# Performance work log

Measured on AMD Instinct MI355X. Metric: run time of the kernel, lower is better.

## Reference

```python
import jax, jax.numpy as jnp
from jax import lax
import numpy as np


def _bn(x, g, b, eps=1e-5):
    # BatchNorm2d in training mode: biased batch stats over (N,H,W) per channel
    m = jnp.mean(x, axis=(0, 2, 3), keepdims=True)
    v = jnp.mean((x - m) ** 2, axis=(0, 2, 3), keepdims=True)
    return (x - m) * lax.rsqrt(v + eps) * g[None, :, None, None] + b[None, :, None, None]


def _conv(x, w, b, pad):
    y = lax.conv_general_dilated(x, w, (1, 1), [(pad, pad), (pad, pad)],
                                 dimension_numbers=('NCHW', 'OIHW', 'NCHW'))
    return y + b[None, :, None, None]


def _prelu(x, a):
    return jnp.where(x >= 0, x, a * x)


def _maxpool2(x):
    return lax.reduce_window(x, -jnp.inf, lax.max, (1, 1, 2, 2), (1, 1, 2, 2), 'VALID')


def _up2(x):
    # UpsamplingBilinear2d(scale_factor=2) -> bilinear, align_corners=True
    B, C, H, W = x.shape
    def idx(n):
        pos = jnp.arange(2 * n, dtype=x.dtype) * (n - 1) / (2 * n - 1)
        lo = jnp.floor(pos).astype(jnp.int32)
        hi = jnp.minimum(lo + 1, n - 1)
        return lo, hi, pos - lo.astype(x.dtype)
    lo, hi, f = idx(H)
    x = x[:, :, lo, :] * (1 - f)[:, None] + x[:, :, hi, :] * f[:, None]
    lo, hi, f = idx(W)
    x = x[:, :, :, lo] * (1 - f) + x[:, :, :, hi] * f
    return x


def _forward(x, n16, sigma16, bias16, prelu_a,
             bn3_g, bn3_b, bn32_g, bn32_b, bn64_g, bn64_b, bn128_g, bn128_b,
             w1, b1, w2, b2, w3, b3, w4, b4, w5, b5, w6, b6, w7, b7, w11, b11):
    B, C, H, W = x.shape
    # 16 enhancement curves fused: r_k = x^{n_k} / (x^{n_k} + sigma_k^{n_k} + bias_k)
    xn = x[None] ** n16[:, None, None, None, None]          # (16,B,3,H,W)
    r = xn / (xn + (sigma16 ** n16)[:, None, None, None, None]
              + bias16[:, None, None, None, None])
    # each branch gets its own BatchNorm2d(3) stats (same affine params)
    r = jax.vmap(lambda t: _bn(t, bn3_g, bn3_b))(r)
    x_fusion = jnp.transpose(r, (1, 0, 2, 3, 4)).reshape(B, 16 * C, H, W)
    x1 = _bn(_maxpool2(_prelu(_conv(x_fusion, w1, b1, 1), prelu_a)), bn32_g, bn32_b)
    x2 = _bn(_maxpool2(_prelu(_conv(x1, w2, b2, 1), prelu_a)), bn64_g, bn64_b)
    x3 = _bn(_maxpool2(_prelu(_conv(x2, w3, b3, 1), prelu_a)), bn128_g, bn128_b)
    x4 = _bn(_conv(x3, w4, b4, 1), bn128_g, bn128_b)
    x5 = _bn(_up2(_prelu(_conv(jnp.concatenate([x4, x3], 1), w5, b5, 1), prelu_a)), bn64_g, bn64_b)
    x6 = _bn(_up2(_prelu(_conv(jnp.concatenate([x2, x5], 1), w6, b6, 1), prelu_a)), bn32_g, bn32_b)
    x_out = jax.nn.sigmoid(_up2(_prelu(_conv(jnp.concatenate([x1, x6], 1), w7, b7, 1), prelu_a)))
    x_out = _conv(x_out, w11, b11, 0)
    x_mean = jnp.mean(x, axis=1, keepdims=True)
    x_out1 = jnp.mean(x_out, axis=1, keepdims=True)
    return x_out1 * (x / (x_mean + 1e-6))


def setup_inputs() -> dict:
    key = jax.random.key(0)
    ks = jax.random.split(key, 16)
    B, H, W = 8, 256, 256
    nf = 32
    x = jax.random.uniform(ks[0], (B, 3, H, W), jnp.float32, 1e-3, 1.0)
    n16 = jnp.arange(1, 17, dtype=jnp.float32) * 0.5
    sigma16 = jnp.full((16,), 0.5, jnp.float32)
    bias16 = jnp.full((16,), 1e-4, jnp.float32)
    prelu_a = jnp.float32(0.25)
    def cw(k, o, i, kk):
        return jax.random.normal(k, (o, i, kk, kk), jnp.float32) * 0.05
    def cb(o):
        return jnp.zeros((o,), jnp.float32)
    return dict(
        x=x, n16=n16, sigma16=sigma16, bias16=bias16, prelu_a=prelu_a,
        bn3_g=jnp.ones((3,), jnp.float32), bn3_b=jnp.zeros((3,), jnp.float32),
        bn32_g=jnp.ones((32,), jnp.float32), bn32_b=jnp.zeros((32,), jnp.float32),
        bn64_g=jnp.ones((64,), jnp.float32), bn64_b=jnp.zeros((64,), jnp.float32),
        bn128_g=jnp.ones((128,), jnp.float32), bn128_b=jnp.zeros((128,), jnp.float32),
        w1=cw(ks[1], nf, 48, 3), b1=cb(nf),
        w2=cw(ks[2], 2 * nf, nf, 3), b2=cb(2 * nf),
        w3=cw(ks[3], 4 * nf, 2 * nf, 3), b3=cb(4 * nf),
        w4=cw(ks[4], 4 * nf, 4 * nf, 3), b4=cb(4 * nf),
        w5=cw(ks[5], 2 * nf, 8 * nf, 3), b5=cb(2 * nf),
        w6=cw(ks[6], nf, 4 * nf, 3), b6=cb(nf),
        w7=cw(ks[7], nf, 2 * nf, 3), b7=cb(nf),
        w11=cw(ks[8], 3, nf, 1), b11=cb(3),
    )


def reference(x, n16, sigma16, bias16, prelu_a,
              bn3_g, bn3_b, bn32_g, bn32_b, bn64_g, bn64_b, bn128_g, bn128_b,
              w1, b1, w2, b2, w3, b3, w4, b4, w5, b5, w6, b6, w7, b7, w11, b11):
    return _forward(x, n16, sigma16, bias16, prelu_a,
                    bn3_g, bn3_b, bn32_g, bn32_b, bn64_g, bn64_b, bn128_g, bn128_b,
                    w1, b1, w2, b2, w3, b3, w4, b4, w5, b5, w6, b6, w7, b7, w11, b11)
```

## Files before the change

kernel.cpp:

```cpp
#include <hip/hip_runtime.h>

#define FAST_EXP2(x) __builtin_amdgcn_exp2f(x)
#define FAST_LOG2(x) __builtin_amdgcn_logf(x)
#define FAST_RCP(x)  __builtin_amdgcn_rcpf(x)

static constexpr size_t S3_SUM=0,   S3_SQ=48;
static constexpr size_t S32A_SUM=96,  S32A_SQ=128;
static constexpr size_t S64A_SUM=160, S64A_SQ=224;
static constexpr size_t S128A_SUM=288,S128A_SQ=416;
static constexpr size_t S128B_SUM=544,S128B_SQ=672;
static constexpr size_t S64B_SUM=800, S64B_SQ=864;
static constexpr size_t S32B_SUM=928, S32B_SQ=960;
static constexpr size_t A3_=1024,  B3_=1072;
static constexpr size_t A32A_=1120, B32A_=1152;
static constexpr size_t A64A_=1184, B64A_=1248;
static constexpr size_t A128A_=1312,B128A_=1440;
static constexpr size_t A128B_=1568,B128B_=1696;
static constexpr size_t A64B_=1824, B64B_=1888;
static constexpr size_t A32B_=1952, B32B_=1984;
static constexpr size_t SPB_=2016, WBAR_=2032, BBAR_=2064;
static constexpr size_t T1_=4096;
static constexpr size_t T2_=T1_+4194304;
static constexpr size_t T3_=T2_+2097152;
static constexpr size_t T4_=T3_+1048576;
static constexpr size_t C5_=T4_+1048576;
static constexpr size_t U5_=C5_+524288;
static constexpr size_t C6_=U5_+2097152;
static constexpr size_t U6_=C6_+1048576;
static constexpr size_t C7_=U6_+4194304;
static constexpr size_t W1S_=C7_+4194304;
static constexpr size_t B1S_=W1S_+13824;
static constexpr size_t PAD_=B1S_+64;

__global__ void k_precomp(const float* __restrict__ n16, const float* __restrict__ sig16,
                          const float* __restrict__ b16, const float* __restrict__ w11,
                          const float* __restrict__ b11,
                          float* __restrict__ spb, float* __restrict__ wbar, float* __restrict__ bbar)
{
    int t = threadIdx.x;
    if (t < 16) spb[t] = powf(sig16[t], n16[t]) + b16[t];
    else if (t < 48) { int j = t - 16; wbar[j] = (w11[j] + w11[32 + j] + w11[64 + j]) * (1.f/3.f); }
    else if (t == 48) bbar[0] = (b11[0] + b11[1] + b11[2]) * (1.f/3.f);
}

__global__ __launch_bounds__(256) void k_branch_stats(
    const float* __restrict__ x, const float* __restrict__ n16,
    const float* __restrict__ sig16, const float* __restrict__ b16,
    float* __restrict__ sum, float* __restrict__ sq)
{
    const int c = blockIdx.x >> 6;
    const int chunk = blockIdx.x & 63;
    float nk[16], den[16];
#pragma unroll
    for (int k = 0; k < 16; ++k) { nk[k] = n16[k]; den[k] = powf(sig16[k], nk[k]) + b16[k]; }
    float s[16], q[16];
#pragma unroll
    for (int k = 0; k < 16; ++k) { s[k] = 0.f; q[k] = 0.f; }
    const int per = 8192;
    int start = chunk * per;
    for (int i = start + (int)threadIdx.x; i < start + per; i += 256) {
        int b = i >> 16, hw = i & 65535;
        float xv = x[(size_t)(b*3 + c)*65536 + hw];
        float t = FAST_LOG2(xv);
#pragma unroll
        for (int k = 0; k < 16; ++k) {
            float v = FAST_EXP2(nk[k]*t);
            float r = v * FAST_RCP(v + den[k]);
            s[k] += r; q[k] += r*r;
        }
    }
    __shared__ float red[4][32];
    int lane = threadIdx.x & 63, wid = threadIdx.x >> 6;
#pragma unroll
    for (int k = 0; k < 16; ++k) {
#pragma unroll
        for (int off = 32; off > 0; off >>= 1) {
            s[k] += __shfl_down(s[k], off);
            q[k] += __shfl_down(q[k], off);
        }
    }
    if (lane == 0) {
#pragma unroll
        for (int k = 0; k < 16; ++k) { red[wid][k] = s[k]; red[wid][16+k] = q[k]; }
    }
    __syncthreads();
    if (threadIdx.x < 32) {
        float v = red[0][threadIdx.x] + red[1][threadIdx.x] + red[2][threadIdx.x] + red[3][threadIdx.x];
        int k = threadIdx.x & 15;
        if (threadIdx.x < 16) atomicAdd(&sum[k*3 + c], v);
        else                  atomicAdd(&sq[k*3 + c], v);
    }
}

__global__ __launch_bounds__(256) void k_stats(
    const float* __restrict__ in, int C, int HW, int nchunks, int per,
    float* __restrict__ sum, float* __restrict__ sq)
{
    int c = blockIdx.x / nchunks;
    int chunk = blockIdx.x - c*nchunks;
    float s = 0.f, q = 0.f;
    int start = chunk * per, end = start + per;
    for (int i = start + (int)threadIdx.x; i < end; i += 256) {
        int b = i / HW, hw = i - b*HW;
        float v = in[((size_t)b*C + c)*HW + hw];
        s += v; q += v*v;
    }
#pragma unroll
    for (int off = 32; off > 0; off >>= 1) { s += __shfl_down(s, off); q += __shfl_down(q, off); }
    __shared__ float ss[4], qq[4];
    int lane = threadIdx.x & 63, wid = threadIdx.x >> 6;
    if (lane == 0) { ss[wid] = s; qq[wid] = q; }
    __syncthreads();
    if (threadIdx.x == 0) {
        atomicAdd(&sum[c], ss[0]+ss[1]+ss[2]+ss[3]);
        atomicAdd(&sq[c],  qq[0]+qq[1]+qq[2]+qq[3]);
    }
}

__global__ void k_finalize(const float* __restrict__ sum, const float* __restrict__ sq,
                           const float* __restrict__ g, const float* __restrict__ bb,
                           int C, int gdim, float invN,
                           float* __restrict__ A, float* __restrict__ Bs)
{
    int i = blockIdx.x*blockDim.x + threadIdx.x;
    if (i < C) {
        float m   = sum[i]*invN;
        float var = fmaxf(sq[i]*invN - m*m, 0.f);
        float inv = rsqrtf(var + 1e-5f);
        float a   = g[i % gdim]*inv;
        A[i]  = a;
        Bs[i] = bb[i % gdim] - m*a;
    }
}

__global__ __launch_bounds__(256) void k_finalize_fill(
    const float* __restrict__ sum, const float* __restrict__ sq,
    const float* __restrict__ g, const float* __restrict__ bb,
    int C, int gdim, float invN,
    float* __restrict__ A, float* __restrict__ Bs,
    const float* __restrict__ fbias, float* __restrict__ fout, int fC, int fHW, int ftotal)
{
    if (blockIdx.x == 0 && threadIdx.x < (unsigned)C) {
        int i = threadIdx.x;
        float m   = sum[i]*invN;
        float var = fmaxf(sq[i]*invN - m*m, 0.f);
        float inv = rsqrtf(var + 1e-5f);
        float a   = g[i % gdim]*inv;
        A[i]  = a;
        Bs[i] = bb[i % gdim] - m*a;
    }
    int idx = blockIdx.x*256 + threadIdx.x;
    if (idx < ftotal) {
        int c = (idx / fHW) % fC;
        fout[idx] = fbias[c];
    }
}

__global__ __launch_bounds__(256) void k_prep1(
    const float* __restrict__ w1, const float* __restrict__ b1,
    const float* __restrict__ A3, const float* __restrict__ B3,
    float* __restrict__ w1s, float* __restrict__ b1s, float* __restrict__ padg)
{
    int tid = threadIdx.x;
    for (int t = tid; t < 13824; t += 256) {
        int ci = (t / 9) % 48;
        w1s[t] = w1[t] * A3[ci];
    }
    if (tid < 48) padg[tid] = -B3[tid] * FAST_RCP(A3[tid]);
    if (tid < 32) {
        float s = b1[tid];
        const float* wp = w1 + tid*432;
        for (int i = 0; i < 432; ++i) s += wp[i] * B3[i/9];
        b1s[tid] = s;
    }
}

template<int COG>
__device__ inline void stats_reduce8(float (&ssum)[COG], float (&ssq)[COG],
                                     float (*redst)[16], int cob,
                                     float* __restrict__ gsum, float* __restrict__ gsq)
{
    int lane = threadIdx.x & 63, wid = threadIdx.x >> 6;
#pragma unroll
    for (int co = 0; co < COG; ++co) {
#pragma unroll
        for (int off = 32; off > 0; off >>= 1) {
            ssum[co] += __shfl_down(ssum[co], off);
            ssq[co]  += __shfl_down(ssq[co],  off);
        }
    }
    if (lane == 0) {
#pragma unroll
        for (int co = 0; co < COG; ++co) { redst[wid][co] = ssum[co]; redst[wid][8+co] = ssq[co]; }
    }
    __syncthreads();
    if (threadIdx.x < 16) {
        float v = redst[0][threadIdx.x] + redst[1][threadIdx.x] + redst[2][threadIdx.x] + redst[3][threadIdx.x];
        if (threadIdx.x < 8) atomicAdd(&gsum[cob + threadIdx.x], v);
        else                 atomicAdd(&gsq[cob + threadIdx.x - 8], v);
    }
}

template<int COG>
__global__ __launch_bounds__(256,2) void k_conv1f(
    const float* __restrict__ x,
    const float* __restrict__ n16, const float* __restrict__ spb,
    const float* __restrict__ w1s, const float* __restrict__ b1s,
    const float* __restrict__ padg,
    const float* __restrict__ prelu_a,
    float* __restrict__ out, float* __restrict__ gsum, float* __restrict__ gsq)
{
    const int tx = threadIdx.x & 15, ty = threadIdx.x >> 4;
    const int nco = 32 / COG;
    const int b = blockIdx.z / nco, cob = (blockIdx.z - b*nco)*COG;
    const int x0 = blockIdx.x*32, y0 = blockIdx.y*32;

    __shared__ float wl[COG*48*9];
    __shared__ float tl[3*1224];
    __shared__ float nl[16], dl[16], padl[48];
    __shared__ float redst[4][16];

    for (int t = threadIdx.x; t < COG*48*9; t += 256) {
        int co = t % COG; int rest = t / COG;
        int kk = rest % 9; int ci = rest / 9;
        wl[t] = w1s[(((size_t)(cob+co))*48 + ci)*9 + kk];
    }
    if (threadIdx.x < 16)       nl[threadIdx.x]      = n16[threadIdx.x];
    else if (threadIdx.x < 32)  dl[threadIdx.x-16]   = spb[threadIdx.x-16];
    else if (threadIdx.x < 80)  padl[threadIdx.x-32] = padg[threadIdx.x-32];

#pragma unroll
    for (int j = 0; j < 14; ++j) {
        int i = threadIdx.x + 256*j;
        if (i < 3468) {
            int ch = i / 1156, jj = i - ch*1156;
            int rr = jj / 34, cc = jj - rr*34;
            int gy = y0 - 1 + rr, gx = x0 - 1 + cc;
            float tv = 0.f;
            if ((unsigned)gy < 256u && (unsigned)gx < 256u)
                tv = FAST_LOG2(x[((size_t)(b*3+ch))*65536 + gy*256 + gx]);
            tl[ch*1224 + rr*36 + cc] = tv;
        }
    }
    __syncthreads();

    float ivt[3][16];
#pragma unroll
    for (int ch = 0; ch < 3; ++ch) {
        const float* tlp = &tl[ch*1224 + (2*ty)*36 + 2*tx];
#pragma unroll
        for (int r = 0; r < 4; ++r) {
            float2 a2 = *(const float2*)(tlp + r*36);
            float2 b2 = *(const float2*)(tlp + r*36 + 2);
            ivt[ch][r*4+0]=a2.x; ivt[ch][r*4+1]=a2.y; ivt[ch][r*4+2]=b2.x; ivt[ch][r*4+3]=b2.y;
        }
    }
    unsigned mask = 0;
#pragma unroll
    for (int r = 0; r < 4; ++r)
#pragma unroll
        for (int c = 0; c < 4; ++c) {
            int gy = y0 + 2*ty - 1 + r, gx = x0 + 2*tx - 1 + c;
            if ((unsigned)gy < 256u && (unsigned)gx < 256u) mask |= 1u << (r*4+c);
        }

    float acc[COG][4];
#pragma unroll
    for (int i = 0; i < COG; ++i)
#pragma unroll
        for (int j = 0; j < 4; ++j) acc[i][j] = 0.f;

#pragma unroll 1
    for (int k = 0; k < 16; ++k) {
        float nk = nl[k], dk = dl[k];
#pragma unroll
        for (int ch = 0; ch < 3; ++ch) {
            float pv = padl[k*3 + ch];
            float rr_[16];
#pragma unroll
            for (int e = 0; e < 16; ++e) {
                float v = FAST_EXP2(nk * ivt[ch][e]);
                float rv = v * FAST_RCP(v + dk);
                rr_[e] = ((mask >> e) & 1u) ? rv : pv;
            }
            const float* wbase = &wl[((k*3+ch)*9)*COG];
#pragma unroll
            for (int kh = 0; kh < 3; ++kh)
#pragma unroll
            for (int kw = 0; kw < 3; ++kw) {
                const int kk = kh*3 + kw;
                float wv[COG];
#pragma unroll
                for (int q = 0; q < COG/4; ++q) {
                    float4 wq = *((const float4*)(wbase + kk*COG) + q);
                    wv[4*q+0]=wq.x; wv[4*q+1]=wq.y; wv[4*q+2]=wq.z; wv[4*q+3]=wq.w;
                }
#pragma unroll
                for (int co = 0; co < COG; ++co)
#pragma unroll
                    for (int py = 0; py < 2; ++py)
#pragma unroll
                        for (int px = 0; px < 2; ++px)
                            acc[co][py*2+px] += wv[co]*rr_[(py+kh)*4 + (px+kw)];
            }
        }
    }

    float a = __ldg(prelu_a);
    int pyp = (y0 >> 1) + ty, pxp = (x0 >> 1) + tx;
    float ssum[COG], ssq[COG];
#pragma unroll
    for (int co = 0; co < COG; ++co) {
        float bv = b1s[cob + co];
        float v0 = acc[co][0] + bv, v1 = acc[co][1] + bv;
        float v2 = acc[co][2] + bv, v3 = acc[co][3] + bv;
        v0 = v0 >= 0.f ? v0 : a*v0; v1 = v1 >= 0.f ? v1 : a*v1;
        v2 = v2 >= 0.f ? v2 : a*v2; v3 = v3 >= 0.f ? v3 : a*v3;
        float m = fmaxf(fmaxf(v0,v1), fmaxf(v2,v3));
        out[(((size_t)b*32 + cob + co)*128 + pyp)*128 + pxp] = m;
        ssum[co] = m; ssq[co] = m*m;
    }
    __syncthreads();
    stats_reduce8<COG>(ssum, ssq, redst, cob, gsum, gsq);
}

template<int COG, bool POOL>
__global__ __launch_bounds__(256,2) void k_conv_big(
    const float* __restrict__ in1, int C1,
    const float* __restrict__ sc1, const float* __restrict__ sh1,
    const float* __restrict__ w, const float* __restrict__ bias,
    int Cout, int H, int W, const float* __restrict__ prelu_a, int do_prelu,
    float* __restrict__ out, float* __restrict__ gsum, float* __restrict__ gsq)
{
    const int Cin = C1;
    const int tx = threadIdx.x & 15, ty = threadIdx.x >> 4;
    const int nco = Cout / COG;
    const int b = blockIdx.z / nco, cob = (blockIdx.z - b*nco)*COG;
    const int x0 = blockIdx.x*64, y0 = blockIdx.y*32;

    __shared__ float wl[COG*64*9];
    __shared__ float tile[2][34*68];
    __shared__ float redst[4][16];

    for (int t = threadIdx.x; t < COG*Cin*9; t += 256) {
        int co = t % COG; int rest = t / COG;
        int k = rest % 9; int ci = rest / 9;
        wl[t] = w[(((size_t)(cob+co))*Cin + ci)*9 + k];
    }

    float acc[COG][8];
#pragma unroll
    for (int i = 0; i < COG; ++i)
#pragma unroll
        for (int j = 0; j < 8; ++j) acc[i][j] = 0.f;

#pragma unroll 1
    for (int cb = 0; cb < Cin; cb += 2) {
#pragma unroll
        for (int sub = 0; sub < 2; ++sub) {
            int ci = cb + sub;
            float scv = sc1 ? sc1[ci] : 1.f;
            float shv = sc1 ? sh1[ci] : 0.f;
            const float* base = in1 + ((size_t)b*Cin + ci)*H*W;
#pragma unroll 1
            for (int i = threadIdx.x; i < 34*66; i += 256) {
                int r = i / 66, c = i - r*66;
                int gy = y0 - 1 + r, gx = x0 - 1 + c;
                float v = 0.f;
                if ((unsigned)gy < (unsigned)H && (unsigned)gx < (unsigned)W)
                    v = base[(size_t)gy*W + gx]*scv + shv;
                tile[sub][r*68 + c] = v;
            }
        }
        __syncthreads();
#pragma unroll
        for (int sub = 0; sub < 2; ++sub) {
            const float* tl = &tile[sub][(2*ty)*68 + 4*tx];
            float iv[4][6];
#pragma unroll
            for (int r = 0; r < 4; ++r) {
                float4 av = *(const float4*)(tl + r*68);
                float2 bv = *(const float2*)(tl + r*68 + 4);
                iv[r][0]=av.x; iv[r][1]=av.y; iv[r][2]=av.z; iv[r][3]=av.w;
                iv[r][4]=bv.x; iv[r][5]=bv.y;
            }
            const float* wbase = &wl[(cb+sub)*9*COG];
#pragma unroll
            for (int kh = 0; kh < 3; ++kh)
#pragma unroll
            for (int kw = 0; kw < 3; ++kw) {
                const int k = kh*3 + kw;
                float wv[COG];
#pragma unroll
                for (int q = 0; q < COG/4; ++q) {
                    float4 wq = *((const float4*)(wbase + k*COG) + q);
                    wv[4*q+0]=wq.x; wv[4*q+1]=wq.y; wv[4*q+2]=wq.z; wv[4*q+3]=wq.w;
                }
#pragma unroll
                for (int co = 0; co < COG; ++co)
#pragma unroll
                    for (int py = 0; py < 2; ++py)
#pragma unroll
                        for (int px = 0; px < 4; ++px)
                            acc[co][py*4+px] += wv[co]*iv[py+kh][px+kw];
            }
        }
        __syncthreads();
    }

    float a = __ldg(prelu_a);
    float ssum[COG], ssq[COG];
    if (POOL) {
        const int Hp = H >> 1, Wp = W >> 1;
        int pyp = (y0 >> 1) + ty, pxp = (x0 >> 1) + 2*tx;
#pragma unroll
        for (int co = 0; co < COG; ++co) {
            float bv = bias[cob + co];
            float v[8];
#pragma unroll
            for (int p = 0; p < 8; ++p) {
                float t = acc[co][p] + bv;
                v[p] = t >= 0.f ? t : a*t;
            }
            float2 st;
            st.x = fmaxf(fmaxf(v[0], v[1]), fmaxf(v[4], v[5]));
            st.y = fmaxf(fmaxf(v[2], v[3]), fmaxf(v[6], v[7]));
            *(float2*)(out + (((size_t)b*Cout + cob + co)*Hp + pyp)*Wp + pxp) = st;
            ssum[co] = st.x + st.y; ssq[co] = st.x*st.x + st.y*st.y;
        }
        stats_reduce8<COG>(ssum, ssq, redst, cob, gsum, gsq);
    } else {
        int oy = y0 + 2*ty, ox = x0 + 4*tx;
#pragma unroll
        for (int co = 0; co < COG; ++co) {
            float bv = bias[cob + co];
            float* op = out + (((size_t)b*Cout + cob + co)*H + oy)*W + ox;
#pragma unroll
            for (int py = 0; py < 2; ++py) {
                float4 st;
                float t0 = acc[co][py*4+0] + bv, t1 = acc[co][py*4+1] + bv;
                float t2 = acc[co][py*4+2] + bv, t3 = acc[co][py*4+3] + bv;
                if (do_prelu) {
                    t0 = t0 >= 0.f ? t0 : a*t0; t1 = t1 >= 0.f ? t1 : a*t1;
                    t2 = t2 >= 0.f ? t2 : a*t2; t3 = t3 >= 0.f ? t3 : a*t3;
                }
                st.x=t0; st.y=t1; st.z=t2; st.w=t3;
                *(float4*)(op + py*W) = st;
            }
        }
    }
}

template<int COG, int MAXCI, bool POOL, bool SPLIT, bool STATS>
__global__ __launch_bounds__(256,2) void k_conv32(
    const float* __restrict__ in1, int C1,
    const float* __restrict__ sc1, const float* __restrict__ sh1,
    const float* __restrict__ in2, int C2,
    const float* __restrict__ sc2, const float* __restrict__ sh2,
    const float* __restrict__ w, const float* __restrict__ bias,
    int Cout, int H, int W, const float* __restrict__ prelu_a, int do_prelu,
    int ciN, int nsplit,
    float* __restrict__ out, float* __restrict__ gsum, float* __restrict__ gsq)
{
    const int Cin = C1 + C2;
    const int tx = threadIdx.x & 15, ty = threadIdx.x >> 4;
    const int nco = Cout / COG;
    int z = blockIdx.z;
    const int sp = z % nsplit; z /= nsplit;
    const int b = z / nco, cob = (z - b*nco)*COG;
    const int ci0 = sp * ciN;
    const int x0 = blockIdx.x*32, y0 = blockIdx.y*32;

    __shared__ float wl[COG*MAXCI*9];
    __shared__ float tile[2][34*36];
    __shared__ float redst[4][16];

    for (int t = threadIdx.x; t < COG*ciN*9; t += 256) {
        int co = t % COG; int rest = t / COG;
        int k = rest % 9; int ci = rest / 9;
        wl[t] = w[(((size_t)(cob+co))*Cin + ci0 + ci)*9 + k];
    }

    float acc[COG][4];
#pragma unroll
    for (int i = 0; i < COG; ++i)
#pragma unroll
        for (int j = 0; j < 4; ++j) acc[i][j] = 0.f;

#pragma unroll 1
    for (int cb = 0; cb < ciN; cb += 2) {
#pragma unroll
        for (int sub = 0; sub < 2; ++sub) {
            int ci = ci0 + cb + sub;
            const float* in; int cc; const float* scp; const float* shp; int Cn;
            if (ci < C1) { in = in1; cc = ci;      scp = sc1; shp = sh1; Cn = C1; }
            else         { in = in2; cc = ci - C1; scp = sc2; shp = sh2; Cn = C2; }
            float scv = scp ? scp[cc] : 1.f;
            float shv = scp ? shp[cc] : 0.f;
            const float* base = in + ((size_t)b*Cn + cc)*H*W;
#pragma unroll 1
            for (int i = threadIdx.x; i < 34*34; i += 256) {
                int r = i / 34, c = i - r*34;
                int gy = y0 - 1 + r, gx = x0 - 1 + c;
                float v = 0.f;
                if ((unsigned)gy < (unsigned)H && (unsigned)gx < (unsigned)W)
                    v = base[(size_t)gy*W + gx]*scv + shv;
                tile[sub][r*36 + c] = v;
            }
        }
        __syncthreads();
#pragma unroll
        for (int sub = 0; sub < 2; ++sub) {
            const float* tl = &tile[sub][(2*ty)*36 + 2*tx];
            float iv[4][4];
#pragma unroll
            for (int r = 0; r < 4; ++r) {
                float2 a2 = *(const float2*)(tl + r*36);
                float2 b2 = *(const float2*)(tl + r*36 + 2);
                iv[r][0]=a2.x; iv[r][1]=a2.y; iv[r][2]=b2.x; iv[r][3]=b2.y;
            }
            const float* wbase = &wl[(cb+sub)*9*COG];
#pragma unroll
            for (int kh = 0; kh < 3; ++kh)
#pragma unroll
            for (int kw = 0; kw < 3; ++kw) {
                const int k = kh*3 + kw;
                float wv[COG];
#pragma unroll
                for (int q = 0; q < COG/4; ++q) {
                    float4 wq = *((const float4*)(wbase + k*COG) + q);
                    wv[4*q+0]=wq.x; wv[4*q+1]=wq.y; wv[4*q+2]=wq.z; wv[4*q+3]=wq.w;
                }
#pragma unroll
                for (int co = 0; co < COG; ++co)
#pragma unroll
                    for (int py = 0; py < 2; ++py)
#pragma unroll
                        for (int px = 0; px < 2; ++px)
                            acc[co][py*2+px] += wv[co]*iv[py+kh][px+kw];
            }
        }
        __syncthreads();
    }

    if (SPLIT) {
        int oy = y0 + 2*ty, ox = x0 + 2*tx;
#pragma unroll
        for (int co = 0; co < COG; ++co) {
            float* op = out + (((size_t)b*Cout + cob + co)*H + oy)*W + ox;
            atomicAdd(&op[0],     acc[co][0]);
            atomicAdd(&op[1],     acc[co][1]);
            atomicAdd(&op[W],     acc[co][2]);
            atomicAdd(&op[W + 1], acc[co][3]);
        }
    } else {
        float a = __ldg(prelu_a);
        float ssum[COG], ssq[COG];
        if (POOL) {
            const int Hp = H >> 1, Wp = W >> 1;
            int pyp = (y0 >> 1) + ty, pxp = (x0 >> 1) + tx;
#pragma unroll
            for (int co = 0; co < COG; ++co) {
                float bv = bias[cob + co];
                float v0 = acc[co][0] + bv, v1 = acc[co][1] + bv;
                float v2 = acc[co][2] + bv, v3 = acc[co][3] + bv;
                v0 = v0 >= 0.f ? v0 : a*v0; v1 = v1 >= 0.f ? v1 : a*v1;
                v2 = v2 >= 0.f ? v2 : a*v2; v3 = v3 >= 0.f ? v3 : a*v3;
                float m = fmaxf(fmaxf(v0,v1), fmaxf(v2,v3));
                out[(((size_t)b*Cout + cob + co)*Hp + pyp)*Wp + pxp] = m;
                ssum[co] = m; ssq[co] = m*m;
            }
            if (STATS) stats_reduce8<COG>(ssum, ssq, redst, cob, gsum, gsq);
        } else {
            int oy = y0 + 2*ty, ox = x0 + 2*tx;
#pragma unroll
            for (int co = 0; co < COG; ++co) {
                float bv = bias[cob + co];
                float* op = out + (((size_t)b*Cout + cob + co)*H + oy)*W + ox;
                float v0 = acc[co][0] + bv, v1 = acc[co][1] + bv;
                float v2 = acc[co][2] + bv, v3 = acc[co][3] + bv;
                if (do_prelu) {
                    v0 = v0 >= 0.f ? v0 : a*v0; v1 = v1 >= 0.f ? v1 : a*v1;
                    v2 = v2 >= 0.f ? v2 : a*v2; v3 = v3 >= 0.f ? v3 : a*v3;
                }
                op[0] = v0; op[1] = v1; op[W] = v2; op[W+1] = v3;
                ssum[co] = v0+v1+v2+v3; ssq[co] = v0*v0+v1*v1+v2*v2+v3*v3;
            }
            if (STATS) stats_reduce8<COG>(ssum, ssq, redst, cob, gsum, gsq);
        }
    }
}

__global__ __launch_bounds__(256) void k_up2(
    const float* __restrict__ in, float* __restrict__ out, int C, int h, int w,
    const float* __restrict__ prelu_a, int do_prelu,
    float* __restrict__ gsum, float* __restrict__ gsq)
{
    int idx = blockIdx.x*256 + threadIdx.x;
    int W2 = 2*w, H2 = 2*h;
    float a = do_prelu ? __ldg(prelu_a) : 0.f;
    int ox = idx % W2; int t = idx / W2; int oy = t % H2; int bc = t / H2;
    float py = ((float)oy * (float)(h-1)) / (float)(2*h - 1);
    int ly = (int)floorf(py); int hy = min(ly+1, h-1); float fy = py - (float)ly;
    float px = ((float)ox * (float)(w-1)) / (float)(2*w - 1);
    int lx = (int)floorf(px); int hx = min(lx+1, w-1); float fx = px - (float)lx;
    const float* p = in + (size_t)bc*h*w;
    float v00 = p[(size_t)ly*w + lx], v01 = p[(size_t)ly*w + hx];
    float v10 = p[(size_t)hy*w + lx], v11 = p[(size_t)hy*w + hx];
    if (do_prelu) {
        v00 = v00 >= 0.f ? v00 : a*v00;
        v01 = v01 >= 0.f ? v01 : a*v01;
        v10 = v10 >= 0.f ? v10 : a*v10;
        v11 = v11 >= 0.f ? v11 : a*v11;
    }
    float v0 = v00*(1.f-fx) + v01*fx;
    float v1 = v10*(1.f-fx) + v11*fx;
    float v = v0*(1.f-fy) + v1*fy;
    out[idx] = v;
    float s = v, q = v*v;
#pragma unroll
    for (int off = 32; off > 0; off >>= 1) { s += __shfl_down(s, off); q += __shfl_down(q, off); }
    __shared__ float ss[4], qq[4];
    int lane = threadIdx.x & 63, wid = threadIdx.x >> 6;
    if (lane == 0) { ss[wid] = s; qq[wid] = q; }
    __syncthreads();
    if (threadIdx.x == 0) {
        int c = bc % C;
        atomicAdd(&gsum[c], ss[0]+ss[1]+ss[2]+ss[3]);
        atomicAdd(&gsq[c],  qq[0]+qq[1]+qq[2]+qq[3]);
    }
}

__global__ __launch_bounds__(256) void k_final(
    const float* __restrict__ c7, const float* __restrict__ x,
    const float* __restrict__ wbar, const float* __restrict__ bbar,
    float* __restrict__ out)
{
    int idx = blockIdx.x*256 + threadIdx.x;
    if (idx >= 8*65536) return;
    int hw = idx & 65535, b = idx >> 16;
    int oy = hw >> 8, ox = hw & 255;
    float py = ((float)oy * 127.f) / 255.f;
    int ly = (int)floorf(py); int hy = min(ly+1, 127); float fy = py - (float)ly;
    float px = ((float)ox * 127.f) / 255.f;
    int lx = (int)floorf(px); int hx = min(lx+1, 127); float fx = px - (float)lx;
    float w00 = (1.f-fy)*(1.f-fx), w01 = (1.f-fy)*fx, w10 = fy*(1.f-fx), w11v = fy*fx;
    const float* base = c7 + (size_t)b*32*16384;
    float accum = bbar[0];
#pragma unroll 8
    for (int j = 0; j < 32; ++j) {
        const float* p = base + (size_t)j*16384;
        float v = p[ly*128 + lx]*w00 + p[ly*128 + hx]*w01 + p[hy*128 + lx]*w10 + p[hy*128 + hx]*w11v;
        float s = FAST_RCP(1.f + __expf(-v));
        accum += wbar[j]*s;
    }
    size_t xb = (size_t)b*3*65536 + hw;
    float x0 = x[xb], x1 = x[xb + 65536], x2 = x[xb + 2*65536];
    float m = (x0 + x1 + x2)*(1.f/3.f) + 1e-6f;
    float sc = accum * FAST_RCP(m);
    out[xb]            = sc*x0;
    out[xb + 65536]    = sc*x1;
    out[xb + 2*65536]  = sc*x2;
}

extern "C" void kernel_launch(void* const* d_in, const int* in_sizes, int n_in,
                              void* d_out, int out_size, void* d_ws, size_t ws_size,
                              hipStream_t stream) {
    const float* x       = (const float*)d_in[0];
    const float* n16     = (const float*)d_in[1];
    const float* sig16   = (const float*)d_in[2];
    const float* bia16   = (const float*)d_in[3];
    const float* prelu_a = (const float*)d_in[4];
    const float* bn3_g   = (const float*)d_in[5];
    const float* bn3_b   = (const float*)d_in[6];
    const float* bn32_g  = (const float*)d_in[7];
    const float* bn32_b  = (const float*)d_in[8];
    const float* bn64_g  = (const float*)d_in[9];
    const float* bn64_b  = (const float*)d_in[10];
    const float* bn128_g = (const float*)d_in[11];
    const float* bn128_b = (const float*)d_in[12];
    const float* w1 = (const float*)d_in[13]; const float* b1 = (const float*)d_in[14];
    const float* w2 = (const float*)d_in[15]; const float* b2 = (const float*)d_in[16];
    const float* w3 = (const float*)d_in[17]; const float* b3 = (const float*)d_in[18];
    const float* w4 = (const float*)d_in[19]; const float* b4 = (const float*)d_in[20];
    const float* w5 = (const float*)d_in[21]; const float* b5 = (const float*)d_in[22];
    const float* w6 = (const float*)d_in[23]; const float* b6 = (const float*)d_in[24];
    const float* w7 = (const float*)d_in[25]; const float* b7 = (const float*)d_in[26];
    const float* w11= (const float*)d_in[27]; const float* b11= (const float*)d_in[28];
    float* ws  = (float*)d_ws;
    float* out = (float*)d_out;

    (void)hipMemsetAsync(d_ws, 0, 4096*sizeof(float), stream);

    k_precomp<<<1, 64, 0, stream>>>(n16, sig16, bia16, w11, b11, ws+SPB_, ws+WBAR_, ws+BBAR_);

    k_branch_stats<<<192, 256, 0, stream>>>(x, n16, sig16, bia16, ws+S3_SUM, ws+S3_SQ);
    k_finalize<<<1, 128, 0, stream>>>(ws+S3_SUM, ws+S3_SQ, bn3_g, bn3_b, 48, 3, 1.f/524288.f, ws+A3_, ws+B3_);
    k_prep1<<<1, 256, 0, stream>>>(w1, b1, ws+A3_, ws+B3_, ws+W1S_, ws+B1S_, ws+PAD_);

    k_conv1f<8><<<dim3(8,8,32), 256, 0, stream>>>(x, n16, ws+SPB_, ws+W1S_, ws+B1S_, ws+PAD_,
                                                  prelu_a, ws+T1_, ws+S32A_SUM, ws+S32A_SQ);
    k_finalize<<<1, 128, 0, stream>>>(ws+S32A_SUM, ws+S32A_SQ, bn32_g, bn32_b, 32, 32, 1.f/131072.f, ws+A32A_, ws+B32A_);

    k_conv_big<8,true><<<dim3(2,4,64), 256, 0, stream>>>(
        ws+T1_, 32, ws+A32A_, ws+B32A_, w2, b2, 64, 128, 128, prelu_a, 1,
        ws+T2_, ws+S64A_SUM, ws+S64A_SQ);
    k_finalize<<<1, 128, 0, stream>>>(ws+S64A_SUM, ws+S64A_SQ, bn64_g, bn64_b, 64, 64, 1.f/32768.f, ws+A64A_, ws+B64A_);

    k_conv32<8,64,true,false,true><<<dim3(2,2,128), 256, 0, stream>>>(
        ws+T2_, 64, ws+A64A_, ws+B64A_, nullptr, 0, nullptr, nullptr,
        w3, b3, 128, 64, 64, prelu_a, 1, 64, 1, ws+T3_, ws+S128A_SUM, ws+S128A_SQ);
    k_finalize_fill<<<4096, 256, 0, stream>>>(ws+S128A_SUM, ws+S128A_SQ, bn128_g, bn128_b,
                                              128, 128, 1.f/8192.f, ws+A128A_, ws+B128A_,
                                              b4, ws+T4_, 128, 1024, 1048576);

    k_conv32<8,32,false,true,false><<<dim3(1,1,512), 256, 0, stream>>>(
        ws+T3_, 128, ws+A128A_, ws+B128A_, nullptr, 0, nullptr, nullptr,
        w4, nullptr, 128, 32, 32, prelu_a, 0, 32, 4, ws+T4_, nullptr, nullptr);
    k_stats<<<512, 256, 0, stream>>>(ws+T4_, 128, 1024, 4, 2048, ws+S128B_SUM, ws+S128B_SQ);
    k_finalize_fill<<<2048, 256, 0, stream>>>(ws+S128B_SUM, ws+S128B_SQ, bn128_g, bn128_b,
                                              128, 128, 1.f/8192.f, ws+A128B_, ws+B128B_,
                                              b5, ws+C5_, 64, 1024, 524288);

    k_conv32<8,32,false,true,false><<<dim3(1,1,512), 256, 0, stream>>>(
        ws+T4_, 128, ws+A128B_, ws+B128B_, ws+T3_, 128, ws+A128A_, ws+B128A_,
        w5, nullptr, 64, 32, 32, prelu_a, 0, 32, 8, ws+C5_, nullptr, nullptr);
    k_up2<<<8192, 256, 0, stream>>>(ws+C5_, ws+U5_, 64, 32, 32, prelu_a, 1, ws+S64B_SUM, ws+S64B_SQ);
    k_finalize_fill<<<4096, 256, 0, stream>>>(ws+S64B_SUM, ws+S64B_SQ, bn64_g, bn64_b,
                                              64, 64, 1.f/32768.f, ws+A64B_, ws+B64B_,
                                              b6, ws+C6_, 32, 4096, 1048576);

    k_conv32<8,32,false,true,false><<<dim3(2,2,128), 256, 0, stream>>>(
        ws+T2_, 64, ws+A64A_, ws+B64A_, ws+U5_, 64, ws+A64B_, ws+B64B_,
        w6, nullptr, 32, 64, 64, prelu_a, 0, 32, 4, ws+C6_, nullptr, nullptr);
    k_up2<<<16384, 256, 0, stream>>>(ws+C6_, ws+U6_, 32, 64, 64, prelu_a, 1, ws+S32B_SUM, ws+S32B_SQ);
    k_finalize<<<1, 128, 0, stream>>>(ws+S32B_SUM, ws+S32B_SQ, bn32_g, bn32_b, 32, 32, 1.f/131072.f, ws+A32B_, ws+B32B_);

    k_conv32<8,64,false,false,false><<<dim3(4,4,32), 256, 0, stream>>>(
        ws+T1_, 32, ws+A32A_, ws+B32A_, ws+U6_, 32, ws+A32B_, ws+B32B_,
        w7, b7, 32, 128, 128, prelu_a, 1, 64, 1, ws+C7_, nullptr, nullptr);

    k_final<<<2048, 256, 0, stream>>>(ws+C7_, x, ws+WBAR_, ws+BBAR_, out);
}
```

Measured before the change: 1.485 ms.

## Compute curve transforms once per tile pixel into double-buffered shared memory

Before, each thread evaluated the exp2/rcp enhancement curve for its own overlapping 4x4 halo window, so neighbouring threads recomputed the same pixels many times. Now each thread keeps the log2 of the pixels it loaded in registers. For each of the 16 curves it computes the transform once per tile pixel and writes it into a double-buffered shared tile. The next curve's transform is produced while the current curve's convolution runs. This removes the redundant transcendental work, at the cost of extra LDS writes and reads, a block barrier per curve, and more shared memory that could lower occupancy.

```diff
diff --git a/kernel.cpp b/kernel.cpp
--- a/kernel.cpp
+++ b/kernel.cpp
@@ -216,8 +216,8 @@
     const int x0 = blockIdx.x*32, y0 = blockIdx.y*32;
 
     __shared__ float wl[COG*48*9];
-    __shared__ float tl[3*1224];
-    __shared__ float nl[16], dl[16], padl[48];
+    __shared__ float rl[2][3*1224];
+    __shared__ float nl16[16], dl16[16], padl[48];
     __shared__ float redst[4][16];
 
     for (int t = threadIdx.x; t < COG*48*9; t += 256) {
@@ -225,10 +225,12 @@
         int kk = rest % 9; int ci = rest / 9;
         wl[t] = w1s[(((size_t)(cob+co))*48 + ci)*9 + kk];
     }
-    if (threadIdx.x < 16)       nl[threadIdx.x]      = n16[threadIdx.x];
-    else if (threadIdx.x < 32)  dl[threadIdx.x-16]   = spb[threadIdx.x-16];
+    if (threadIdx.x < 16)       nl16[threadIdx.x]    = n16[threadIdx.x];
+    else if (threadIdx.x < 32)  dl16[threadIdx.x-16] = spb[threadIdx.x-16];
     else if (threadIdx.x < 80)  padl[threadIdx.x-32] = padg[threadIdx.x-32];
 
+    float tlr[14];
+    int off_[14]; int chpack = 0; int okf = 0;
 #pragma unroll
     for (int j = 0; j < 14; ++j) {
         int i = threadIdx.x + 256*j;
@@ -236,52 +238,59 @@
             int ch = i / 1156, jj = i - ch*1156;
             int rr = jj / 34, cc = jj - rr*34;
             int gy = y0 - 1 + rr, gx = x0 - 1 + cc;
-            float tv = 0.f;
-            if ((unsigned)gy < 256u && (unsigned)gx < 256u)
-                tv = FAST_LOG2(x[((size_t)(b*3+ch))*65536 + gy*256 + gx]);
-            tl[ch*1224 + rr*36 + cc] = tv;
+            bool ok = (unsigned)gy < 256u && (unsigned)gx < 256u;
+            off_[j] = ch*1224 + rr*36 + cc;
+            chpack |= ch << (2*j);
+            tlr[j] = 0.f;
+            if (ok) {
+                okf |= 1 << j;
+                tlr[j] = FAST_LOG2(x[((size_t)(b*3+ch))*65536 + gy*256 + gx]);
+            }
+        } else { off_[j] = 3671; tlr[j] = 0.f; }
+    }
+
+    float acc[COG][4];
+#pragma unroll
+    for (int i = 0; i < COG; ++i)
+#pragma unroll
+        for (int j = 0; j < 4; ++j) acc[i][j] = 0.f;
+
+    {
+        float nk = nl16[0], dk = dl16[0];
+#pragma unroll
+        for (int j = 0; j < 14; ++j) {
+            int ch = (chpack >> (2*j)) & 3;
+            float pv = padl[ch];
+            float v = FAST_EXP2(nk * tlr[j]);
+            float rv = v * FAST_RCP(v + dk);
+            rl[0][off_[j]] = ((okf >> j) & 1) ? rv : pv;
         }
     }
     __syncthreads();
-
-    float ivt[3][16];
-#pragma unroll
-    for (int ch = 0; ch < 3; ++ch) {
-        const float* tlp = &tl[ch*1224 + (2*ty)*36 + 2*tx];
-#pragma unroll
-        for (int r = 0; r < 4; ++r) {
-            float2 a2 = *(const float2*)(tlp + r*36);
-            float2 b2 = *(const float2*)(tlp + r*36 + 2);
-            ivt[ch][r*4+0]=a2.x; ivt[ch][r*4+1]=a2.y; ivt[ch][r*4+2]=b2.x; ivt[ch][r*4+3]=b2.y;
-        }
-    }
-    unsigned mask = 0;
-#pragma unroll
-    for (int r = 0; r < 4; ++r)
-#pragma unroll
-        for (int c = 0; c < 4; ++c) {
-            int gy = y0 + 2*ty - 1 + r, gx = x0 + 2*tx - 1 + c;
-            if ((unsigned)gy < 256u && (unsigned)gx < 256u) mask |= 1u << (r*4+c);
-        }
-
-    float acc[COG][4];
-#pragma unroll
-    for (int i = 0; i < COG; ++i)
-#pragma unroll
-        for (int j = 0; j < 4; ++j) acc[i][j] = 0.f;
 
 #pragma unroll 1
     for (int k = 0; k < 16; ++k) {
-        float nk = nl[k], dk = dl[k];
+        if (k < 15) {
+            float nk = nl16[k+1], dk = dl16[k+1];
+#pragma unroll
+            for (int j = 0; j < 14; ++j) {
+                int ch = (chpack >> (2*j)) & 3;
+                float pv = padl[(k+1)*3 + ch];
+                float v = FAST_EXP2(nk * tlr[j]);
+                float rv = v * FAST_RCP(v + dk);
+                rl[(k+1)&1][off_[j]] = ((okf >> j) & 1) ? rv : pv;
+            }
+        }
+        const float* rbuf = rl[k&1];
 #pragma unroll
         for (int ch = 0; ch < 3; ++ch) {
-            float pv = padl[k*3 + ch];
-            float rr_[16];
-#pragma unroll
-            for (int e = 0; e < 16; ++e) {
-                float v = FAST_EXP2(nk * ivt[ch][e]);
-                float rv = v * FAST_RCP(v + dk);
-                rr_[e] = ((mask >> e) & 1u) ? rv : pv;
+            const float* tlp = rbuf + ch*1224 + (2*ty)*36 + 2*tx;
+            float iv[4][4];
+#pragma unroll
+            for (int r = 0; r < 4; ++r) {
+                float2 a2 = *(const float2*)(tlp + r*36);
+                float2 b2 = *(const float2*)(tlp + r*36 + 2);
+                iv[r][0]=a2.x; iv[r][1]=a2.y; iv[r][2]=b2.x; iv[r][3]=b2.y;
             }
             const float* wbase = &wl[((k*3+ch)*9)*COG];
 #pragma unroll
@@ -301,9 +310,10 @@
                     for (int py = 0; py < 2; ++py)
 #pragma unroll
                         for (int px = 0; px < 2; ++px)
-                            acc[co][py*2+px] += wv[co]*rr_[(py+kh)*4 + (px+kw)];
-            }
-        }
+                            acc[co][py*2+px] += wv[co]*iv[py+kh][px+kw];
+            }
+        }
+        __syncthreads();
     }
 
     float a = __ldg(prelu_a);
```

Measured after the change: 1.389 ms. 6.4% less time.
